# Performance work log

Measured on AMD Instinct MI355X. Metric: run time of the kernel, lower is better.

The kernel has to match this reference:

```python
import jax, jax.numpy as jnp
import numpy as np

NUM_GRAPHS = 16384


def setup_inputs() -> dict:
    key = jax.random.key(0)
    k1, k2, k3, k4 = jax.random.split(key, 4)
    N, C = 1000000, 128
    x = jax.random.normal(k1, (N, C), dtype=jnp.float32)
    batch = jnp.sort(jax.random.randint(k2, (N,), 0, NUM_GRAPHS)).astype(jnp.int64)
    # Linear weights, kaiming-ish scale
    gate_w = jax.random.normal(k3, (C, 1), dtype=jnp.float32) * (1.0 / np.sqrt(C))
    gate_b = jnp.zeros((1,), dtype=jnp.float32)
    nn_w = jax.random.normal(k4, (C, 2 * C), dtype=jnp.float32) * (1.0 / np.sqrt(C))
    nn_b = jnp.zeros((2 * C,), dtype=jnp.float32)
    return {"x": x, "batch": batch, "gate_w": gate_w, "gate_b": gate_b,
            "nn_w": nn_w, "nn_b": nn_b}


def reference(x, batch, gate_w, gate_b, nn_w, nn_b):
    # gate_nn: [N, C] -> [N, 1]
    gate = (x @ gate_w + gate_b)[:, 0]            # [N]
    # nn: [N, C] -> [N, 2C]
    h = x @ nn_w + nn_b                           # [N, 2C]
    # per-graph (segment) softmax over gate scores
    m = jax.ops.segment_max(gate, batch, num_segments=NUM_GRAPHS)   # [B]
    e = jnp.exp(gate - m[batch])                                    # [N]
    s = jax.ops.segment_sum(e, batch, num_segments=NUM_GRAPHS)      # [B]
    w = e / s[batch]                                                # [N]
    # weighted scatter-sum: [B, 2C]
    out = jax.ops.segment_sum(h * w[:, None], batch, num_segments=NUM_GRAPHS)
    return out
```

## Files before the change

kernel.cpp:

```cpp
#include <hip/hip_runtime.h>

#define NUM_GRAPHS 16384
#define C 128
#define G 16

__device__ __forceinline__ int lb(const int* __restrict__ a, int n, int v, int lo) {
    int hi = n;
    while (lo < hi) {
        int m = (lo + hi) >> 1;
        if (a[m] < v) lo = m + 1; else hi = m;
    }
    return lo;
}

__global__ __launch_bounds__(256) void segment_pool_kernel(
    const float* __restrict__ x,
    const int*   __restrict__ batch,
    const float* __restrict__ gate_w,
    float*       __restrict__ y,
    float*       __restrict__ s,
    int N)
{
    const int w    = (blockIdx.x * blockDim.x + threadIdx.x) >> 6;
    const int lane = threadIdx.x & 63;
    const int g    = lane >> 4;
    const int t    = lane & 15;
    if (w >= NUM_GRAPHS) return;

    const int start = lb(batch, N, w, 0);
    const int end   = lb(batch, N, w + 1, start);

    const float4* __restrict__ gw4 = (const float4*)(gate_w + t * 8);
    const float4 gwa = gw4[0];
    const float4 gwb = gw4[1];

    float acc[8] = {0.f, 0.f, 0.f, 0.f, 0.f, 0.f, 0.f, 0.f};
    float se = 0.f;

    for (int r = start + g; r < end; r += 4) {
        const float4* __restrict__ xp = (const float4*)(x + (size_t)r * C + t * 8);
        float4 a = xp[0];
        float4 b = xp[1];

        float p = a.x * gwa.x + a.y * gwa.y + a.z * gwa.z + a.w * gwa.w
                + b.x * gwb.x + b.y * gwb.y + b.z * gwb.z + b.w * gwb.w;
        p += __shfl_xor(p, 1, 64);
        p += __shfl_xor(p, 2, 64);
        p += __shfl_xor(p, 4, 64);
        p += __shfl_xor(p, 8, 64);
        float e = __expf(p);

        acc[0] += e * a.x; acc[1] += e * a.y;
        acc[2] += e * a.z; acc[3] += e * a.w;
        acc[4] += e * b.x; acc[5] += e * b.y;
        acc[6] += e * b.z; acc[7] += e * b.w;
        se += e;
    }

    #pragma unroll
    for (int k = 0; k < 8; ++k) {
        acc[k] += __shfl_xor(acc[k], 16, 64);
        acc[k] += __shfl_xor(acc[k], 32, 64);
    }
    se += __shfl_xor(se, 16, 64);
    se += __shfl_xor(se, 32, 64);

    if (g == 0) {
        float4* __restrict__ yp = (float4*)(y + (size_t)w * C + t * 8);
        yp[0] = make_float4(acc[0], acc[1], acc[2], acc[3]);
        yp[1] = make_float4(acc[4], acc[5], acc[6], acc[7]);
        if (t == 0) s[w] = se;
    }
}

__global__ __launch_bounds__(256) void finalize_kernel(
    const float* __restrict__ y,
    const float* __restrict__ s,
    const float* __restrict__ nn_w,
    const float* __restrict__ nn_b,
    float*       __restrict__ out)
{
    const int j  = threadIdx.x;
    const int b0 = blockIdx.x * G;

    __shared__ float ysh[G * C];
    __shared__ float ssh[G];

    for (int idx = threadIdx.x; idx < G * C; idx += 256) {
        int gg = idx >> 7;
        float sv = s[b0 + gg];
        ysh[idx] = (sv > 0.f) ? y[(size_t)b0 * C + idx] / sv : 0.f;
    }
    if (threadIdx.x < G) ssh[threadIdx.x] = s[b0 + threadIdx.x];
    __syncthreads();

    float acc[G];
    #pragma unroll
    for (int gg = 0; gg < G; ++gg) acc[gg] = 0.f;

    #pragma unroll 4
    for (int c = 0; c < C; ++c) {
        float wv = nn_w[c * 256 + j];
        #pragma unroll
        for (int gg = 0; gg < G; ++gg)
            acc[gg] += ysh[gg * C + c] * wv;
    }

    const float bias = nn_b[j];
    #pragma unroll
    for (int gg = 0; gg < G; ++gg)
        out[(size_t)(b0 + gg) * 256 + j] = (ssh[gg] > 0.f) ? acc[gg] + bias : 0.f;
}

extern "C" void kernel_launch(void* const* d_in, const int* in_sizes, int n_in,
                              void* d_out, int out_size, void* d_ws, size_t ws_size,
                              hipStream_t stream) {
    const float* x      = (const float*)d_in[0];
    const int*   batch  = (const int*)d_in[1];
    const float* gate_w = (const float*)d_in[2];
    const float* nn_w   = (const float*)d_in[4];
    const float* nn_b   = (const float*)d_in[5];
    float* out = (float*)d_out;
    const int N = in_sizes[1];

    float* y = (float*)d_ws;
    float* s = y + (size_t)NUM_GRAPHS * C;

    segment_pool_kernel<<<NUM_GRAPHS / 4, 256, 0, stream>>>(x, batch, gate_w, y, s, N);

    finalize_kernel<<<NUM_GRAPHS / G, 256, 0, stream>>>(y, s, nn_w, nn_b, out);
}
```

Measured before the change: 714.2 us.

## Precompute segment offsets, unroll row loop by four, coalesce x loads

Adds a pass over the sorted batch array that writes each graph's start offset, replacing two per-wave binary searches over a million-element array. The pooling loop now processes four rows per iteration to raise memory-level parallelism. Each 16-lane group reads two contiguous 256-byte halves of a row instead of 32-byte chunks per lane, for better coalescing. This costs an extra kernel launch and a read of batch, and graphs with no nodes rely on the boundary-fill logic.

```diff
diff --git a/kernel.cpp b/kernel.cpp
--- a/kernel.cpp
+++ b/kernel.cpp
@@ -4,18 +4,31 @@
 #define C 128
 #define G 16
 
-__device__ __forceinline__ int lb(const int* __restrict__ a, int n, int v, int lo) {
-    int hi = n;
-    while (lo < hi) {
-        int m = (lo + hi) >> 1;
-        if (a[m] < v) lo = m + 1; else hi = m;
-    }
-    return lo;
+__global__ __launch_bounds__(256) void build_segstart_kernel(
+    const int* __restrict__ batch, int* __restrict__ seg_start, int N)
+{
+    int i = blockIdx.x * blockDim.x + threadIdx.x;
+    if (i >= N) return;
+    int cur  = batch[i];
+    int prev = (i == 0) ? -1 : batch[i - 1];
+    for (int w = prev + 1; w <= cur; ++w) seg_start[w] = i;
+    if (i == N - 1)
+        for (int w = cur + 1; w <= NUM_GRAPHS; ++w) seg_start[w] = N;
+}
+
+__device__ __forceinline__ float row_e(float4 a, float4 b, float4 gwa, float4 gwb) {
+    float p = a.x * gwa.x + a.y * gwa.y + a.z * gwa.z + a.w * gwa.w
+            + b.x * gwb.x + b.y * gwb.y + b.z * gwb.z + b.w * gwb.w;
+    p += __shfl_xor(p, 1, 64);
+    p += __shfl_xor(p, 2, 64);
+    p += __shfl_xor(p, 4, 64);
+    p += __shfl_xor(p, 8, 64);
+    return __expf(p);
 }
 
 __global__ __launch_bounds__(256) void segment_pool_kernel(
     const float* __restrict__ x,
-    const int*   __restrict__ batch,
+    const int*   __restrict__ seg_start,
     const float* __restrict__ gate_w,
     float*       __restrict__ y,
     float*       __restrict__ s,
@@ -27,48 +40,62 @@
     const int t    = lane & 15;
     if (w >= NUM_GRAPHS) return;
 
-    const int start = lb(batch, N, w, 0);
-    const int end   = lb(batch, N, w + 1, start);
+    const int start = seg_start[w];
+    const int end   = seg_start[w + 1];
 
-    const float4* __restrict__ gw4 = (const float4*)(gate_w + t * 8);
-    const float4 gwa = gw4[0];
-    const float4 gwb = gw4[1];
+    const float4 gwa = *(const float4*)(gate_w + t * 4);
+    const float4 gwb = *(const float4*)(gate_w + 64 + t * 4);
 
-    float acc[8] = {0.f, 0.f, 0.f, 0.f, 0.f, 0.f, 0.f, 0.f};
+    float ax = 0.f, ay = 0.f, az = 0.f, aw = 0.f;
+    float bx = 0.f, by = 0.f, bz = 0.f, bw = 0.f;
     float se = 0.f;
 
-    for (int r = start + g; r < end; r += 4) {
-        const float4* __restrict__ xp = (const float4*)(x + (size_t)r * C + t * 8);
-        float4 a = xp[0];
-        float4 b = xp[1];
-
-        float p = a.x * gwa.x + a.y * gwa.y + a.z * gwa.z + a.w * gwa.w
-                + b.x * gwb.x + b.y * gwb.y + b.z * gwb.z + b.w * gwb.w;
-        p += __shfl_xor(p, 1, 64);
-        p += __shfl_xor(p, 2, 64);
-        p += __shfl_xor(p, 4, 64);
-        p += __shfl_xor(p, 8, 64);
-        float e = __expf(p);
-
-        acc[0] += e * a.x; acc[1] += e * a.y;
-        acc[2] += e * a.z; acc[3] += e * a.w;
-        acc[4] += e * b.x; acc[5] += e * b.y;
-        acc[6] += e * b.z; acc[7] += e * b.w;
+    int r = start + g;
+    for (; r + 12 < end; r += 16) {
+        const float4* p0 = (const float4*)(x + (size_t)(r     ) * C) + t;
+        const float4* p1 = (const float4*)(x + (size_t)(r +  4) * C) + t;
+        const float4* p2 = (const float4*)(x + (size_t)(r +  8) * C) + t;
+        const float4* p3 = (const float4*)(x + (size_t)(r + 12) * C) + t;
+        float4 a0 = p0[0], b0 = p0[16];
+        float4 a1 = p1[0], b1 = p1[16];
+        float4 a2 = p2[0], b2 = p2[16];
+        float4 a3 = p3[0], b3 = p3[16];
+        float e0 = row_e(a0, b0, gwa, gwb);
+        float e1 = row_e(a1, b1, gwa, gwb);
+        float e2 = row_e(a2, b2, gwa, gwb);
+        float e3 = row_e(a3, b3, gwa, gwb);
+        ax += e0 * a0.x + e1 * a1.x + e2 * a2.x + e3 * a3.x;
+        ay += e0 * a0.y + e1 * a1.y + e2 * a2.y + e3 * a3.y;
+        az += e0 * a0.z + e1 * a1.z + e2 * a2.z + e3 * a3.z;
+        aw += e0 * a0.w + e1 * a1.w + e2 * a2.w + e3 * a3.w;
+        bx += e0 * b0.x + e1 * b1.x + e2 * b2.x + e3 * b3.x;
+        by += e0 * b0.y + e1 * b1.y + e2 * b2.y + e3 * b3.y;
+        bz += e0 * b0.z + e1 * b1.z + e2 * b2.z + e3 * b3.z;
+        bw += e0 * b0.w + e1 * b1.w + e2 * b2.w + e3 * b3.w;
+        se += e0 + e1 + e2 + e3;
+    }
+    for (; r < end; r += 4) {
+        const float4* p = (const float4*)(x + (size_t)r * C) + t;
+        float4 a = p[0], b = p[16];
+        float e = row_e(a, b, gwa, gwb);
+        ax += e * a.x; ay += e * a.y; az += e * a.z; aw += e * a.w;
+        bx += e * b.x; by += e * b.y; bz += e * b.z; bw += e * b.w;
         se += e;
     }
 
     #pragma unroll
-    for (int k = 0; k < 8; ++k) {
-        acc[k] += __shfl_xor(acc[k], 16, 64);
-        acc[k] += __shfl_xor(acc[k], 32, 64);
+    for (int m = 16; m <= 32; m <<= 1) {
+        ax += __shfl_xor(ax, m, 64); ay += __shfl_xor(ay, m, 64);
+        az += __shfl_xor(az, m, 64); aw += __shfl_xor(aw, m, 64);
+        bx += __shfl_xor(bx, m, 64); by += __shfl_xor(by, m, 64);
+        bz += __shfl_xor(bz, m, 64); bw += __shfl_xor(bw, m, 64);
+        se += __shfl_xor(se, m, 64);
     }
-    se += __shfl_xor(se, 16, 64);
-    se += __shfl_xor(se, 32, 64);
 
     if (g == 0) {
-        float4* __restrict__ yp = (float4*)(y + (size_t)w * C + t * 8);
-        yp[0] = make_float4(acc[0], acc[1], acc[2], acc[3]);
-        yp[1] = make_float4(acc[4], acc[5], acc[6], acc[7]);
+        float4* yp = (float4*)(y + (size_t)w * C);
+        yp[t]      = make_float4(ax, ay, az, aw);
+        yp[t + 16] = make_float4(bx, by, bz, bw);
         if (t == 0) s[w] = se;
     }
 }
@@ -125,8 +152,11 @@
 
     float* y = (float*)d_ws;
     float* s = y + (size_t)NUM_GRAPHS * C;
+    int* seg_start = (int*)(s + NUM_GRAPHS);
 
-    segment_pool_kernel<<<NUM_GRAPHS / 4, 256, 0, stream>>>(x, batch, gate_w, y, s, N);
+    build_segstart_kernel<<<(N + 255) / 256, 256, 0, stream>>>(batch, seg_start, N);
+
+    segment_pool_kernel<<<NUM_GRAPHS / 4, 256, 0, stream>>>(x, seg_start, gate_w, y, s, N);
 
     finalize_kernel<<<NUM_GRAPHS / G, 256, 0, stream>>>(y, s, nn_w, nn_b, out);
 }
```

Result: no change. 702.8 us (-1.6%).
